# Performance work log

Measured on AMD Instinct MI355X. Metric: run time of the kernel, lower is better.

The kernel has to match this reference:

```python
import jax, jax.numpy as jnp
import numpy as np

N, D = 8192, 128

def _rbf_kernel(x, y):
    # InfoVAE-style kernel: exp(-mean((x_i - y_j)^2) / dim) = exp(-sqdist / dim^2)
    dim = x.shape[1]
    x2 = jnp.sum(x * x, axis=1)              # [n]
    y2 = jnp.sum(y * y, axis=1)              # [m]
    sqdist = x2[:, None] + y2[None, :] - 2.0 * (x @ y.T)  # [n, m]
    return jnp.exp(-sqdist / (dim * dim))


def setup_inputs() -> dict:
    key = jax.random.key(0)
    k1, k2 = jax.random.split(key)
    inputs = jax.random.normal(k1, (N, D), dtype=jnp.float32)
    true_samples = jax.random.normal(k2, (N, D), dtype=jnp.float32)
    return {"inputs": inputs, "true_samples": true_samples}


def reference(inputs, true_samples):
    x = true_samples  # samples from standard normal prior
    y = inputs
    k_xx = _rbf_kernel(x, x)
    k_yy = _rbf_kernel(y, y)
    k_xy = _rbf_kernel(x, y)
    mmd = jnp.mean(k_xx) + jnp.mean(k_yy) - 2.0 * jnp.mean(k_xy)
    return mmd
```

## Files before the change

### kernel.cpp

```cpp
#include <hip/hip_runtime.h>
#include <hip/hip_bf16.h>
#include <math.h>


#define NN 8192
#define DD 128
#define TZ 16384
#define TILES 128
#define NBLOCKS (TILES * (TILES + 1) / 2)

typedef __attribute__((ext_vector_type(8))) short bf16x8;
typedef __attribute__((ext_vector_type(4))) float f32x4;
typedef __attribute__((ext_vector_type(2))) float f32x2;

#if __has_builtin(__builtin_amdgcn_exp2f)
#define EXP2F __builtin_amdgcn_exp2f
#else
#define EXP2F exp2f
#endif

constexpr float LOG2E = 0x1.715476p+0f;
constexpr float S2 = LOG2E / 8192.0f;

constexpr int PANEL = 16384;

constexpr size_t WS_NORM = 768;
constexpr size_t WS_Z    = WS_NORM + (size_t)TZ * sizeof(float);

__device__ __forceinline__ void gload_lds16(const void* g, void* l) {
  __builtin_amdgcn_global_load_lds(
      (const __attribute__((address_space(1))) void*)g,
      (__attribute__((address_space(3))) void*)l, 16, 0, 0);
}

__global__ __launch_bounds__(256) void prep(
    const float* __restrict__ X, const float* __restrict__ Y,
    __hip_bfloat16* __restrict__ Z, float* __restrict__ normZ,
    double* __restrict__ sums) {
  if (blockIdx.x == 0 && threadIdx.x < 64) sums[threadIdx.x] = 0.0;

  const int row = blockIdx.x * 4 + (threadIdx.x >> 6);
  const int lane = threadIdx.x & 63;
  const float* __restrict__ src =
      (row < NN) ? (X + (size_t)row * DD) : (Y + (size_t)(row - NN) * DD);
  const float2 v = *reinterpret_cast<const float2*>(src + 2 * lane);

  float n = v.x * v.x + v.y * v.y;
  *reinterpret_cast<__hip_bfloat162*>(Z + (size_t)row * DD + 2 * lane) =
      __hip_bfloat162{__float2bfloat16(v.x), __float2bfloat16(v.y)};

#pragma unroll
  for (int o = 32; o > 0; o >>= 1) n += __shfl_down(n, o);
  if (lane == 0) normZ[row] = n * (-LOG2E / 16384.0f);
}

__device__ __forceinline__ int tri_start(int i) {
  return i * TILES - (i * (i - 1)) / 2;
}

__global__ __launch_bounds__(256, 4) void mmd_mfma(
    const __hip_bfloat16* __restrict__ Z, const float* __restrict__ normZ,
    double* __restrict__ sums) {
  __shared__ alignas(16) char lds[2 * PANEL + 1024];
  __shared__ float rowN[128], colN[128];
  __shared__ double red[4];

  const int t = blockIdx.x;
  int I = (int)((257.0 - sqrt(257.0 * 257.0 - 8.0 * (double)t)) * 0.5);
  if (I > 127) I = 127;
  if (I < 0) I = 0;
  while (I < 127 && tri_start(I + 1) <= t) ++I;
  while (I > 0 && tri_start(I) > t) --I;
  const int J = I + (t - tri_start(I));

  const int tid = threadIdx.x;
  const int lane = tid & 63, wave = tid >> 6;
  const int wr = wave >> 1, wc = wave & 1;
  const int lr = lane & 15, quad = lane >> 4;

  if (tid < 128) rowN[tid] = normZ[I * 128 + tid];
  else           colN[tid - 128] = normZ[J * 128 + tid - 128];

  const char* Zb = (const char*)Z;
  const int r5 = tid >> 3;
  const int g = (tid & 7) ^ (r5 & 7);
  const char* gA = Zb + (size_t)I * 32768 + r5 * 256 + g * 16;
  const char* gB = Zb + (size_t)J * 32768 + r5 * 256 + g * 16;
  char* lw = lds + wave * 1024;

  const int aBase = (wr * 64 + lr) * 128;
  const int bBase = PANEL + (wc * 64 + lr) * 128;
  const int sa = lr & 7;

  f32x4 acc[4][4] = {};
#pragma unroll
  for (int p = 0; p < 2; ++p) {
    __syncthreads();
#pragma unroll
    for (int l = 0; l < 4; ++l) {
      gload_lds16(gA + p * 128 + l * 8192, lw + l * 4096);
      gload_lds16(gB + p * 128 + l * 8192, lw + PANEL + l * 4096);
    }
    __syncthreads();

#pragma unroll
    for (int ks = 0; ks < 2; ++ks) {
      const int csw = (((ks * 4) + quad) ^ sa) * 16;
      bf16x8 a[4], b[4];
#pragma unroll
      for (int i = 0; i < 4; ++i) {
        a[i] = *reinterpret_cast<const bf16x8*>(&lds[aBase + i * 2048 + csw]);
        b[i] = *reinterpret_cast<const bf16x8*>(&lds[bBase + i * 2048 + csw]);
      }
#pragma unroll
      for (int i = 0; i < 4; ++i)
#pragma unroll
        for (int j = 0; j < 4; ++j)
          acc[i][j] = __builtin_amdgcn_mfma_f32_16x16x32_bf16(a[i], b[j], acc[i][j], 0, 0, 0);
    }
  }

  const f32x2 s2v = {S2, S2};
  f32x2 part01 = {0.f, 0.f}, part23 = {0.f, 0.f};
#pragma unroll
  for (int i = 0; i < 4; ++i) {
    const int rbase = wr * 64 + i * 16 + quad * 4;
    const f32x2 ar01 = {rowN[rbase + 0], rowN[rbase + 1]};
    const f32x2 ar23 = {rowN[rbase + 2], rowN[rbase + 3]};
#pragma unroll
    for (int j = 0; j < 4; ++j) {
      const float rb = colN[wc * 64 + j * 16 + lr];
      const f32x2 rb2 = {rb, rb};
      const f32x2 base01 = ar01 + rb2;
      const f32x2 base23 = ar23 + rb2;
      const f32x2 acc01 = {acc[i][j][0], acc[i][j][1]};
      const f32x2 acc23 = {acc[i][j][2], acc[i][j][3]};
      const f32x2 arg01 = __builtin_elementwise_fma(acc01, s2v, base01);
      const f32x2 arg23 = __builtin_elementwise_fma(acc23, s2v, base23);
      part01 += (f32x2){EXP2F(arg01.x), EXP2F(arg01.y)};
      part23 += (f32x2){EXP2F(arg23.x), EXP2F(arg23.y)};
    }
  }
  const f32x2 ps = part01 + part23;
  double local = (double)(ps.x + ps.y);
  double w = ((I < 64) == (J < 64)) ? 1.0 : -1.0;
  if (I != J) w += w;
  local *= w;

#pragma unroll
  for (int o = 32; o > 0; o >>= 1) local += __shfl_down(local, o);
  if (lane == 0) red[wave] = local;
  __syncthreads();
  if (tid == 0) atomicAdd(&sums[t & 63], red[0] + red[1] + red[2] + red[3]);
}

__global__ void finish(const double* __restrict__ s, float* __restrict__ out) {
  double v = s[threadIdx.x];
#pragma unroll
  for (int o = 32; o > 0; o >>= 1) v += __shfl_down(v, o);
  if (threadIdx.x == 0)
    out[0] = (float)(v * (1.0 / ((double)NN * (double)NN)));
}

extern "C" void kernel_launch(void* const* d_in, const int* in_sizes, int n_in,
                              void* d_out, int out_size, void* d_ws, size_t ws_size,
                              hipStream_t stream) {
  const float* y_inputs = (const float*)d_in[0];
  const float* x_true   = (const float*)d_in[1];
  float* out = (float*)d_out;

  char* ws = (char*)d_ws;
  double* sums = (double*)ws;
  float* normZ = (float*)(ws + WS_NORM);
  __hip_bfloat16* Z = (__hip_bfloat16*)(ws + WS_Z);

  prep<<<TZ / 4, 256, 0, stream>>>(x_true, y_inputs, Z, normZ, sums);
  mmd_mfma<<<NBLOCKS, 256, 0, stream>>>(Z, normZ, sums);
  finish<<<1, 64, 0, stream>>>(sums, out);
}
```

Baseline: 112.8 us.

## Load MFMA operands directly from global memory into registers, drop LDS staging

The tile kernel no longer stages A/B panels through shared memory with global_load_lds and barriers. Each wave loads its bf16 fragments straight from global into double-buffered registers, interleaved with the MFMA k-steps. Row and column norms are also read directly from global, and per-wave atomics into 256 slots replace the block-level LDS reduction. Occupancy is lowered to 3 blocks per SM. The aim is to remove LDS traffic and barrier stalls, at the cost of redundant global/L2 loads across waves and higher register pressure.

```diff
diff --git a/kernel.cpp b/kernel.cpp
--- a/kernel.cpp
+++ b/kernel.cpp
@@ -22,22 +22,14 @@
 constexpr float LOG2E = 0x1.715476p+0f;
 constexpr float S2 = LOG2E / 8192.0f;
 
-constexpr int PANEL = 16384;
-
-constexpr size_t WS_NORM = 768;
+constexpr size_t WS_NORM = 2048;
 constexpr size_t WS_Z    = WS_NORM + (size_t)TZ * sizeof(float);
-
-__device__ __forceinline__ void gload_lds16(const void* g, void* l) {
-  __builtin_amdgcn_global_load_lds(
-      (const __attribute__((address_space(1))) void*)g,
-      (__attribute__((address_space(3))) void*)l, 16, 0, 0);
-}
 
 __global__ __launch_bounds__(256) void prep(
     const float* __restrict__ X, const float* __restrict__ Y,
     __hip_bfloat16* __restrict__ Z, float* __restrict__ normZ,
     double* __restrict__ sums) {
-  if (blockIdx.x == 0 && threadIdx.x < 64) sums[threadIdx.x] = 0.0;
+  if (blockIdx.x == 0) sums[threadIdx.x] = 0.0;
 
   const int row = blockIdx.x * 4 + (threadIdx.x >> 6);
   const int lane = threadIdx.x & 63;
@@ -58,13 +50,9 @@
   return i * TILES - (i * (i - 1)) / 2;
 }
 
-__global__ __launch_bounds__(256, 4) void mmd_mfma(
+__global__ __launch_bounds__(256, 3) void mmd_mfma(
     const __hip_bfloat16* __restrict__ Z, const float* __restrict__ normZ,
     double* __restrict__ sums) {
-  __shared__ alignas(16) char lds[2 * PANEL + 1024];
-  __shared__ float rowN[128], colN[128];
-  __shared__ double red[4];
-
   const int t = blockIdx.x;
   int I = (int)((257.0 - sqrt(257.0 * 257.0 - 8.0 * (double)t)) * 0.5);
   if (I > 127) I = 127;
@@ -78,59 +66,66 @@
   const int wr = wave >> 1, wc = wave & 1;
   const int lr = lane & 15, quad = lane >> 4;
 
-  if (tid < 128) rowN[tid] = normZ[I * 128 + tid];
-  else           colN[tid - 128] = normZ[J * 128 + tid - 128];
-
   const char* Zb = (const char*)Z;
-  const int r5 = tid >> 3;
-  const int g = (tid & 7) ^ (r5 & 7);
-  const char* gA = Zb + (size_t)I * 32768 + r5 * 256 + g * 16;
-  const char* gB = Zb + (size_t)J * 32768 + r5 * 256 + g * 16;
-  char* lw = lds + wave * 1024;
-
-  const int aBase = (wr * 64 + lr) * 128;
-  const int bBase = PANEL + (wc * 64 + lr) * 128;
-  const int sa = lr & 7;
+  const char* pA[4];
+  const char* pB[4];
+#pragma unroll
+  for (int i = 0; i < 4; ++i) {
+    pA[i] = Zb + (size_t)(I * 128 + wr * 64 + i * 16 + lr) * 256 + quad * 16;
+    pB[i] = Zb + (size_t)(J * 128 + wc * 64 + i * 16 + lr) * 256 + quad * 16;
+  }
 
   f32x4 acc[4][4] = {};
-#pragma unroll
-  for (int p = 0; p < 2; ++p) {
-    __syncthreads();
-#pragma unroll
-    for (int l = 0; l < 4; ++l) {
-      gload_lds16(gA + p * 128 + l * 8192, lw + l * 4096);
-      gload_lds16(gB + p * 128 + l * 8192, lw + PANEL + l * 4096);
-    }
-    __syncthreads();
+  bf16x8 a[2][4], b[2][4];
 
 #pragma unroll
-    for (int ks = 0; ks < 2; ++ks) {
-      const int csw = (((ks * 4) + quad) ^ sa) * 16;
-      bf16x8 a[4], b[4];
+  for (int i = 0; i < 4; ++i) {
+    a[0][i] = *reinterpret_cast<const bf16x8*>(pA[i]);
+    b[0][i] = *reinterpret_cast<const bf16x8*>(pB[i]);
+  }
+#pragma unroll
+  for (int i = 0; i < 4; ++i) {
+    a[1][i] = *reinterpret_cast<const bf16x8*>(pA[i] + 64);
+    b[1][i] = *reinterpret_cast<const bf16x8*>(pB[i] + 64);
+  }
+
+#pragma unroll
+  for (int ks = 0; ks < 4; ++ks) {
+    const int cur = ks & 1;
+#pragma unroll
+    for (int i = 0; i < 4; ++i)
+#pragma unroll
+      for (int j = 0; j < 4; ++j)
+        acc[i][j] = __builtin_amdgcn_mfma_f32_16x16x32_bf16(
+            a[cur][i], b[cur][j], acc[i][j], 0, 0, 0);
+    if (ks < 2) {
 #pragma unroll
       for (int i = 0; i < 4; ++i) {
-        a[i] = *reinterpret_cast<const bf16x8*>(&lds[aBase + i * 2048 + csw]);
-        b[i] = *reinterpret_cast<const bf16x8*>(&lds[bBase + i * 2048 + csw]);
+        a[cur][i] = *reinterpret_cast<const bf16x8*>(pA[i] + (ks + 2) * 64);
+        b[cur][i] = *reinterpret_cast<const bf16x8*>(pB[i] + (ks + 2) * 64);
       }
-#pragma unroll
-      for (int i = 0; i < 4; ++i)
-#pragma unroll
-        for (int j = 0; j < 4; ++j)
-          acc[i][j] = __builtin_amdgcn_mfma_f32_16x16x32_bf16(a[i], b[j], acc[i][j], 0, 0, 0);
     }
   }
+
+  const float* nzA = normZ + I * 128 + wr * 64;
+  const float* nzB = normZ + J * 128 + wc * 64;
+  f32x4 ar[4];
+  float cb[4];
+#pragma unroll
+  for (int i = 0; i < 4; ++i)
+    ar[i] = *reinterpret_cast<const f32x4*>(nzA + i * 16 + quad * 4);
+#pragma unroll
+  for (int j = 0; j < 4; ++j) cb[j] = nzB[j * 16 + lr];
 
   const f32x2 s2v = {S2, S2};
   f32x2 part01 = {0.f, 0.f}, part23 = {0.f, 0.f};
 #pragma unroll
   for (int i = 0; i < 4; ++i) {
-    const int rbase = wr * 64 + i * 16 + quad * 4;
-    const f32x2 ar01 = {rowN[rbase + 0], rowN[rbase + 1]};
-    const f32x2 ar23 = {rowN[rbase + 2], rowN[rbase + 3]};
+    const f32x2 ar01 = {ar[i].x, ar[i].y};
+    const f32x2 ar23 = {ar[i].z, ar[i].w};
 #pragma unroll
     for (int j = 0; j < 4; ++j) {
-      const float rb = colN[wc * 64 + j * 16 + lr];
-      const f32x2 rb2 = {rb, rb};
+      const f32x2 rb2 = {cb[j], cb[j]};
       const f32x2 base01 = ar01 + rb2;
       const f32x2 base23 = ar23 + rb2;
       const f32x2 acc01 = {acc[i][j][0], acc[i][j][1]};
@@ -149,13 +144,13 @@
 
 #pragma unroll
   for (int o = 32; o > 0; o >>= 1) local += __shfl_down(local, o);
-  if (lane == 0) red[wave] = local;
-  __syncthreads();
-  if (tid == 0) atomicAdd(&sums[t & 63], red[0] + red[1] + red[2] + red[3]);
+  if (lane == 0)
+    atomicAdd(&sums[((t & 63) << 2) | wave], local);
 }
 
 __global__ void finish(const double* __restrict__ s, float* __restrict__ out) {
-  double v = s[threadIdx.x];
+  double v = s[threadIdx.x] + s[threadIdx.x + 64] + s[threadIdx.x + 128] +
+             s[threadIdx.x + 192];
 #pragma unroll
   for (int o = 32; o > 0; o >>= 1) v += __shfl_down(v, o);
   if (threadIdx.x == 0)
```

New measurement: 184.4 us. +63.5%, slower.
